# Optimization experiments

Hardware: AMD Instinct MI355X
Metric: run time of the kernel (lower is better)

## Reference

```python
import jax, jax.numpy as jnp
import numpy as np

MAX_SPAN_WIDTH = 15
NEG_INF = -10000.0


def setup_inputs() -> dict:
    key = jax.random.key(0)
    k1, k2, k3 = jax.random.split(key, 3)
    B, N = 256, 8192
    token_scores = jax.random.normal(k1, (B, N), dtype=jnp.float32)
    attention_mask = jax.random.randint(k2, (B, N), 0, 2, dtype=jnp.int32)
    width_logits = jax.random.normal(k3, (MAX_SPAN_WIDTH,), dtype=jnp.float32)
    gamma = jnp.ones((1,), dtype=jnp.float32)
    return {"token_scores": token_scores, "attention_mask": attention_mask,
            "width_logits": width_logits, "gamma": gamma}


def reference(token_scores, attention_mask, width_logits, gamma):
    B, N = token_scores.shape
    masked = jnp.where(attention_mask == 0, jnp.float32(NEG_INF), token_scores)
    width_weights = jax.nn.softmax(width_logits)  # [MAX_SPAN_WIDTH]
    boost = masked  # width-1 "boost" is the masked scores themselves
    for width in range(2, min(MAX_SPAN_WIDTH + 1, N + 1)):
        # sliding-window min over each width-`width` span -> [B, N-width+1]
        span_mins = jax.lax.reduce_window(
            masked, jnp.inf, jax.lax.min,
            window_dimensions=(1, width), window_strides=(1, 1), padding='VALID')
        w_idx = min(width - 2, MAX_SPAN_WIDTH - 1)
        weighted = span_mins * width_weights[w_idx]
        # max over all offsets a token participates in == sliding-window max
        # over weighted span-mins padded with NEG_INF (matches F.pad(value=NEG_INF))
        padded = jnp.pad(weighted, ((0, 0), (width - 1, width - 1)),
                         constant_values=NEG_INF)  # [B, N+width-1]
        expanded = jax.lax.reduce_window(
            padded, -jnp.inf, jax.lax.max,
            window_dimensions=(1, width), window_strides=(1, 1), padding='VALID')  # [B, N]
        boost = jnp.maximum(boost, expanded)
    return token_scores + gamma * boost
```

## Files before the change

kernel.cpp:

```cpp
#include <hip/hip_runtime.h>
#include <math.h>

#define TPB 256
#define TOK 4
#define TILE (TPB * TOK)
#define HALO 14
#define WIN (TOK + 2 * HALO)
#define NEGINF (-10000.0f)
#define SENT (-1.0e30f)

template <int W>
__device__ __forceinline__ void do_width(const float (&A)[WIN], float wt,
                                         float &b0, float &b1, float &b2,
                                         float &b3) {
  constexpr int K = (W < 4) ? 2 : ((W < 8) ? 4 : 8);
  float Q[W + 3];
#pragma unroll
  for (int u = 0; u < W + 3; ++u) {
    const int s = (HALO + 1) - W + u;
    if constexpr (W == K)
      Q[u] = A[s];
    else
      Q[u] = fminf(A[s], A[s + (W - K)]);
  }
  float m0, m1, m2, m3;
  if constexpr (W == 2) {
    m0 = fmaxf(Q[0], Q[1]);
    m1 = fmaxf(Q[1], Q[2]);
    m2 = fmaxf(Q[2], Q[3]);
    m3 = fmaxf(Q[3], Q[4]);
  } else if constexpr (W == 3) {
    m0 = fmaxf(Q[0], fmaxf(Q[1], Q[2]));
    m1 = fmaxf(Q[1], fmaxf(Q[2], Q[3]));
    m2 = fmaxf(Q[2], fmaxf(Q[3], Q[4]));
    m3 = fmaxf(Q[3], fmaxf(Q[4], Q[5]));
  } else {
    float core = Q[3];
#pragma unroll
    for (int u = 4; u < W; ++u) core = fmaxf(core, Q[u]);
    const float q2c = fmaxf(Q[2], core);
    const float dW = fmaxf(Q[W], Q[W + 1]);
    m0 = fmaxf(fmaxf(Q[0], Q[1]), q2c);
    m1 = fmaxf(fmaxf(Q[1], Q[W]), q2c);
    m2 = fmaxf(q2c, dW);
    m3 = fmaxf(fmaxf(core, Q[W + 2]), dW);
  }
  b0 = fmaxf(b0, m0 * wt);
  b1 = fmaxf(b1, m1 * wt);
  b2 = fmaxf(b2, m2 * wt);
  b3 = fmaxf(b3, m3 * wt);
}

__global__ __launch_bounds__(TPB, 5) void span_kernel(
    const float *__restrict__ ts, const int *__restrict__ mask,
    const float *__restrict__ wlog, const float *__restrict__ gamma_p,
    float *__restrict__ out, int N, int tiles_per_row) {
  __shared__ __align__(16) float sm[TILE + 2 * HALO];
  __shared__ float swt[15];
  const int tid = threadIdx.x;
  const int row = blockIdx.x / tiles_per_row;
  const int t0 = (blockIdx.x % tiles_per_row) * TILE;
  const float *tsrow = ts + (size_t)row * N;
  const int *mrow = mask + (size_t)row * N;

  const int j = tid * TOK;
  const int g = t0 + j;
  const int4 mv = *reinterpret_cast<const int4 *>(&mrow[g]);
  const float4 tv = *reinterpret_cast<const float4 *>(&tsrow[g]);
  {
    float2 w01, w23;
    w01.x = mv.x ? tv.x : NEGINF;
    w01.y = mv.y ? tv.y : NEGINF;
    w23.x = mv.z ? tv.z : NEGINF;
    w23.y = mv.w ? tv.w : NEGINF;
    *reinterpret_cast<float2 *>(&sm[HALO + j]) = w01;
    *reinterpret_cast<float2 *>(&sm[HALO + j + 2]) = w23;
  }
  if (tid < HALO) {
    const int gl = t0 - HALO + tid;
    sm[tid] = (gl >= 0) ? (mrow[gl] ? tsrow[gl] : NEGINF) : SENT;
    const int gr = t0 + TILE + tid;
    sm[TILE + HALO + tid] = (gr < N) ? (mrow[gr] ? tsrow[gr] : NEGINF) : SENT;
  }
  if (tid == TPB - 1) {
    float e[15], mx = -3.4e38f;
#pragma unroll
    for (int i = 0; i < 15; ++i) {
      e[i] = wlog[i];
      mx = fmaxf(mx, e[i]);
    }
    float ssum = 0.0f;
#pragma unroll
    for (int i = 0; i < 15; ++i) {
      e[i] = expf(e[i] - mx);
      ssum += e[i];
    }
    const float inv = 1.0f / ssum;
#pragma unroll
    for (int i = 0; i < 14; ++i) swt[i] = e[i] * inv;
    swt[14] = *gamma_p;
  }
  __syncthreads();

  float A[WIN];
#pragma unroll
  for (int q = 0; q < WIN / 4; ++q) {
    const float4 v = *reinterpret_cast<const float4 *>(&sm[j + 4 * q]);
    A[4 * q + 0] = v.x;
    A[4 * q + 1] = v.y;
    A[4 * q + 2] = v.z;
    A[4 * q + 3] = v.w;
  }
  float b0 = A[HALO + 0], b1 = A[HALO + 1], b2 = A[HALO + 2], b3 = A[HALO + 3];

#pragma unroll
  for (int x = 0; x < WIN - 1; ++x) A[x] = fminf(A[x], A[x + 1]);
  do_width<2>(A, swt[0], b0, b1, b2, b3);
  do_width<3>(A, swt[1], b0, b1, b2, b3);

#pragma unroll
  for (int x = 0; x < WIN - 3; ++x) A[x] = fminf(A[x], A[x + 2]);
  do_width<4>(A, swt[2], b0, b1, b2, b3);
  do_width<5>(A, swt[3], b0, b1, b2, b3);
  do_width<6>(A, swt[4], b0, b1, b2, b3);
  do_width<7>(A, swt[5], b0, b1, b2, b3);

#pragma unroll
  for (int x = 0; x < WIN - 7; ++x) A[x] = fminf(A[x], A[x + 4]);
  do_width<8>(A, swt[6], b0, b1, b2, b3);
  do_width<9>(A, swt[7], b0, b1, b2, b3);
  do_width<10>(A, swt[8], b0, b1, b2, b3);
  do_width<11>(A, swt[9], b0, b1, b2, b3);
  do_width<12>(A, swt[10], b0, b1, b2, b3);
  do_width<13>(A, swt[11], b0, b1, b2, b3);
  do_width<14>(A, swt[12], b0, b1, b2, b3);
  do_width<15>(A, swt[13], b0, b1, b2, b3);

  const float gamma = swt[14];
  float4 o;
  o.x = tv.x + gamma * b0;
  o.y = tv.y + gamma * b1;
  o.z = tv.z + gamma * b2;
  o.w = tv.w + gamma * b3;
  *reinterpret_cast<float4 *>(&out[(size_t)row * N + g]) = o;
}

extern "C" void kernel_launch(void *const *d_in, const int *in_sizes, int n_in,
                              void *d_out, int out_size, void *d_ws,
                              size_t ws_size, hipStream_t stream) {
  const float *ts = (const float *)d_in[0];
  const int *mask = (const int *)d_in[1];
  const float *wlog = (const float *)d_in[2];
  const float *gamma_p = (const float *)d_in[3];
  float *out = (float *)d_out;
  const int N = 8192;
  const int B = in_sizes[0] / N;
  const int tiles = N / TILE;
  span_kernel<<<dim3(B * tiles), dim3(TPB), 0, stream>>>(ts, mask, wlog,
                                                         gamma_p, out, N,
                                                         tiles);
}
```

Before: 14.78 us.

## Swizzle LDS tile, compute softmax weights per-wave via shuffles and readlane

Applies an XOR swizzle to the shared-memory tile indices so the float4 window reads from LDS avoid bank conflicts, padding the buffer to hold the swizzled layout. The softmax over width logits is now computed redundantly by every wave using cross-lane shuffles, and the weights are broadcast with readlane instead of being staged in shared memory by a single thread. This removes a serial single-thread loop and the LDS reads of weights on the critical path. Halo loading is merged into one branch over 28 threads, and launch bounds drop from 5 to 4 waves per SIMD, which may change register allocation and occupancy.

```diff
diff --git a/kernel.cpp b/kernel.cpp
--- a/kernel.cpp
+++ b/kernel.cpp
@@ -8,6 +8,9 @@
 #define WIN (TOK + 2 * HALO)
 #define NEGINF (-10000.0f)
 #define SENT (-1.0e30f)
+#define LDSF 1056
+
+__device__ __forceinline__ int swz(int f) { return f ^ (((f >> 5) & 7) << 2); }
 
 template <int W>
 __device__ __forceinline__ void do_width(const float (&A)[WIN], float wt,
@@ -51,12 +54,13 @@
   b3 = fmaxf(b3, m3 * wt);
 }
 
-__global__ __launch_bounds__(TPB, 5) void span_kernel(
+#define WT(W) __int_as_float(__builtin_amdgcn_readlane(wbits, (W) - 2))
+
+__global__ __launch_bounds__(TPB, 4) void span_kernel(
     const float *__restrict__ ts, const int *__restrict__ mask,
     const float *__restrict__ wlog, const float *__restrict__ gamma_p,
     float *__restrict__ out, int N, int tiles_per_row) {
-  __shared__ __align__(16) float sm[TILE + 2 * HALO];
-  __shared__ float swt[15];
+  __shared__ __align__(16) float sm[LDSF];
   const int tid = threadIdx.x;
   const int row = blockIdx.x / tiles_per_row;
   const int t0 = (blockIdx.x % tiles_per_row) * TILE;
@@ -73,39 +77,39 @@
     w01.y = mv.y ? tv.y : NEGINF;
     w23.x = mv.z ? tv.z : NEGINF;
     w23.y = mv.w ? tv.w : NEGINF;
-    *reinterpret_cast<float2 *>(&sm[HALO + j]) = w01;
-    *reinterpret_cast<float2 *>(&sm[HALO + j + 2]) = w23;
+    const int f0 = HALO + j;
+    *reinterpret_cast<float2 *>(&sm[swz(f0)]) = w01;
+    *reinterpret_cast<float2 *>(&sm[swz(f0 + 2)]) = w23;
   }
-  if (tid < HALO) {
-    const int gl = t0 - HALO + tid;
-    sm[tid] = (gl >= 0) ? (mrow[gl] ? tsrow[gl] : NEGINF) : SENT;
-    const int gr = t0 + TILE + tid;
-    sm[TILE + HALO + tid] = (gr < N) ? (mrow[gr] ? tsrow[gr] : NEGINF) : SENT;
+  if (tid < 2 * HALO) {
+    const int hk = (tid < HALO) ? tid : (TILE + tid);
+    const int tok = t0 - HALO + hk;
+    float v = SENT;
+    if (tok >= 0 && tok < N) v = mrow[tok] ? tsrow[tok] : NEGINF;
+    sm[swz(hk)] = v;
   }
-  if (tid == TPB - 1) {
-    float e[15], mx = -3.4e38f;
+
+  unsigned wbits;
+  {
+    const int li = tid & 15;
+    float v = (li < 15) ? wlog[li] : -3.4e38f;
+    float mx = v;
 #pragma unroll
-    for (int i = 0; i < 15; ++i) {
-      e[i] = wlog[i];
-      mx = fmaxf(mx, e[i]);
-    }
-    float ssum = 0.0f;
+    for (int m = 1; m < 16; m <<= 1) mx = fmaxf(mx, __shfl_xor(mx, m, 64));
+    const float e = expf(v - mx);
+    float s = e;
 #pragma unroll
-    for (int i = 0; i < 15; ++i) {
-      e[i] = expf(e[i] - mx);
-      ssum += e[i];
-    }
-    const float inv = 1.0f / ssum;
-#pragma unroll
-    for (int i = 0; i < 14; ++i) swt[i] = e[i] * inv;
-    swt[14] = *gamma_p;
+    for (int m = 1; m < 16; m <<= 1) s += __shfl_xor(s, m, 64);
+    wbits = __float_as_uint(e / s);
   }
+  const float gamma = *gamma_p;
+
   __syncthreads();
 
   float A[WIN];
 #pragma unroll
   for (int q = 0; q < WIN / 4; ++q) {
-    const float4 v = *reinterpret_cast<const float4 *>(&sm[j + 4 * q]);
+    const float4 v = *reinterpret_cast<const float4 *>(&sm[swz(j + 4 * q)]);
     A[4 * q + 0] = v.x;
     A[4 * q + 1] = v.y;
     A[4 * q + 2] = v.z;
@@ -115,28 +119,27 @@
 
 #pragma unroll
   for (int x = 0; x < WIN - 1; ++x) A[x] = fminf(A[x], A[x + 1]);
-  do_width<2>(A, swt[0], b0, b1, b2, b3);
-  do_width<3>(A, swt[1], b0, b1, b2, b3);
+  do_width<2>(A, WT(2), b0, b1, b2, b3);
+  do_width<3>(A, WT(3), b0, b1, b2, b3);
 
 #pragma unroll
   for (int x = 0; x < WIN - 3; ++x) A[x] = fminf(A[x], A[x + 2]);
-  do_width<4>(A, swt[2], b0, b1, b2, b3);
-  do_width<5>(A, swt[3], b0, b1, b2, b3);
-  do_width<6>(A, swt[4], b0, b1, b2, b3);
-  do_width<7>(A, swt[5], b0, b1, b2, b3);
+  do_width<4>(A, WT(4), b0, b1, b2, b3);
+  do_width<5>(A, WT(5), b0, b1, b2, b3);
+  do_width<6>(A, WT(6), b0, b1, b2, b3);
+  do_width<7>(A, WT(7), b0, b1, b2, b3);
 
 #pragma unroll
   for (int x = 0; x < WIN - 7; ++x) A[x] = fminf(A[x], A[x + 4]);
-  do_width<8>(A, swt[6], b0, b1, b2, b3);
-  do_width<9>(A, swt[7], b0, b1, b2, b3);
-  do_width<10>(A, swt[8], b0, b1, b2, b3);
-  do_width<11>(A, swt[9], b0, b1, b2, b3);
-  do_width<12>(A, swt[10], b0, b1, b2, b3);
-  do_width<13>(A, swt[11], b0, b1, b2, b3);
-  do_width<14>(A, swt[12], b0, b1, b2, b3);
-  do_width<15>(A, swt[13], b0, b1, b2, b3);
+  do_width<8>(A, WT(8), b0, b1, b2, b3);
+  do_width<9>(A, WT(9), b0, b1, b2, b3);
+  do_width<10>(A, WT(10), b0, b1, b2, b3);
+  do_width<11>(A, WT(11), b0, b1, b2, b3);
+  do_width<12>(A, WT(12), b0, b1, b2, b3);
+  do_width<13>(A, WT(13), b0, b1, b2, b3);
+  do_width<14>(A, WT(14), b0, b1, b2, b3);
+  do_width<15>(A, WT(15), b0, b1, b2, b3);
 
-  const float gamma = swt[14];
   float4 o;
   o.x = tv.x + gamma * b0;
   o.y = tv.y + gamma * b1;
```

After: 15.14 us. 1.02x slower.

## Process eight tokens per thread with prefix/suffix max sharing and swizzled LDS

Applied to the files above, without the earlier changes.

Each thread now handles eight tokens instead of four, so the 28-element halo window is amortised over more outputs. The sliding max per width is rebuilt as shared suffix/prefix maxima. The LDS tile gets an XOR swizzle to avoid bank conflicts on the wider float4 reads, and occupancy is lowered to four blocks per CU. The aim is to cut redundant halo loads and min/max work per token, at the cost of more registers and half as many blocks.

```diff
diff --git a/kernel.cpp b/kernel.cpp
--- a/kernel.cpp
+++ b/kernel.cpp
@@ -2,60 +2,80 @@
 #include <math.h>
 
 #define TPB 256
-#define TOK 4
+#define TOK 8
 #define TILE (TPB * TOK)
 #define HALO 14
 #define WIN (TOK + 2 * HALO)
 #define NEGINF (-10000.0f)
 #define SENT (-1.0e30f)
+#define LDSF 2080
+
+__device__ __forceinline__ int swz(int f) { return f ^ (((f >> 5) & 7) << 2); }
 
 template <int W>
 __device__ __forceinline__ void do_width(const float (&A)[WIN], float wt,
-                                         float &b0, float &b1, float &b2,
-                                         float &b3) {
+                                         float (&b)[TOK]) {
   constexpr int K = (W < 4) ? 2 : ((W < 8) ? 4 : 8);
-  float Q[W + 3];
-#pragma unroll
-  for (int u = 0; u < W + 3; ++u) {
-    const int s = (HALO + 1) - W + u;
+  constexpr int S0 = (HALO + 1) - W;
+  constexpr int NQ = W + TOK - 1;
+  float Q[NQ];
+#pragma unroll
+  for (int u = 0; u < NQ; ++u) {
     if constexpr (W == K)
-      Q[u] = A[s];
+      Q[u] = A[S0 + u];
     else
-      Q[u] = fminf(A[s], A[s + (W - K)]);
-  }
-  float m0, m1, m2, m3;
+      Q[u] = fminf(A[S0 + u], A[S0 + u + (W - K)]);
+  }
+  float m[TOK];
   if constexpr (W == 2) {
-    m0 = fmaxf(Q[0], Q[1]);
-    m1 = fmaxf(Q[1], Q[2]);
-    m2 = fmaxf(Q[2], Q[3]);
-    m3 = fmaxf(Q[3], Q[4]);
+#pragma unroll
+    for (int k = 0; k < TOK; ++k) m[k] = fmaxf(Q[k], Q[k + 1]);
   } else if constexpr (W == 3) {
-    m0 = fmaxf(Q[0], fmaxf(Q[1], Q[2]));
-    m1 = fmaxf(Q[1], fmaxf(Q[2], Q[3]));
-    m2 = fmaxf(Q[2], fmaxf(Q[3], Q[4]));
-    m3 = fmaxf(Q[3], fmaxf(Q[4], Q[5]));
+#pragma unroll
+    for (int k = 0; k < TOK; ++k)
+      m[k] = fmaxf(fmaxf(Q[k], Q[k + 1]), Q[k + 2]);
+  } else if constexpr (W < 8) {
+    float SA[4];
+    SA[3] = Q[3];
+#pragma unroll
+    for (int k = 2; k >= 0; --k) SA[k] = fmaxf(Q[k], SA[k + 1]);
+    float TA[W];
+    TA[0] = Q[3];
+#pragma unroll
+    for (int j = 1; j < W; ++j) TA[j] = fmaxf(TA[j - 1], Q[3 + j]);
+#pragma unroll
+    for (int k = 0; k < 4; ++k) m[k] = fmaxf(SA[k], TA[k + W - 4]);
+    float SB[4];
+    SB[3] = Q[7];
+#pragma unroll
+    for (int k = 2; k >= 0; --k) SB[k] = fmaxf(Q[4 + k], SB[k + 1]);
+    float TB[W];
+    TB[0] = Q[7];
+#pragma unroll
+    for (int j = 1; j < W; ++j) TB[j] = fmaxf(TB[j - 1], Q[7 + j]);
+#pragma unroll
+    for (int k = 0; k < 4; ++k) m[4 + k] = fmaxf(SB[k], TB[k + W - 4]);
   } else {
-    float core = Q[3];
-#pragma unroll
-    for (int u = 4; u < W; ++u) core = fmaxf(core, Q[u]);
-    const float q2c = fmaxf(Q[2], core);
-    const float dW = fmaxf(Q[W], Q[W + 1]);
-    m0 = fmaxf(fmaxf(Q[0], Q[1]), q2c);
-    m1 = fmaxf(fmaxf(Q[1], Q[W]), q2c);
-    m2 = fmaxf(q2c, dW);
-    m3 = fmaxf(fmaxf(core, Q[W + 2]), dW);
-  }
-  b0 = fmaxf(b0, m0 * wt);
-  b1 = fmaxf(b1, m1 * wt);
-  b2 = fmaxf(b2, m2 * wt);
-  b3 = fmaxf(b3, m3 * wt);
+    float S[8];
+    S[7] = Q[7];
+#pragma unroll
+    for (int k = 6; k >= 0; --k) S[k] = fmaxf(Q[k], S[k + 1]);
+    float T[W];
+    T[0] = Q[7];
+#pragma unroll
+    for (int j = 1; j < W; ++j) T[j] = fmaxf(T[j - 1], Q[7 + j]);
+#pragma unroll
+    for (int k = 0; k < TOK; ++k) m[k] = fmaxf(S[k], T[k + W - 8]);
+  }
+#pragma unroll
+  for (int k = 0; k < TOK; ++k) b[k] = fmaxf(b[k], m[k] * wt);
 }
 
-__global__ __launch_bounds__(TPB, 5) void span_kernel(
+__global__ __launch_bounds__(TPB, 4) void span_kernel(
     const float *__restrict__ ts, const int *__restrict__ mask,
     const float *__restrict__ wlog, const float *__restrict__ gamma_p,
     float *__restrict__ out, int N, int tiles_per_row) {
-  __shared__ __align__(16) float sm[TILE + 2 * HALO];
+  __shared__ __align__(16) float sm[LDSF];
   __shared__ float swt[15];
   const int tid = threadIdx.x;
   const int row = blockIdx.x / tiles_per_row;
@@ -65,22 +85,33 @@
 
   const int j = tid * TOK;
   const int g = t0 + j;
-  const int4 mv = *reinterpret_cast<const int4 *>(&mrow[g]);
-  const float4 tv = *reinterpret_cast<const float4 *>(&tsrow[g]);
+  const int4 mv0 = *reinterpret_cast<const int4 *>(&mrow[g]);
+  const int4 mv1 = *reinterpret_cast<const int4 *>(&mrow[g + 4]);
+  const float4 tv0 = *reinterpret_cast<const float4 *>(&tsrow[g]);
+  const float4 tv1 = *reinterpret_cast<const float4 *>(&tsrow[g + 4]);
   {
-    float2 w01, w23;
-    w01.x = mv.x ? tv.x : NEGINF;
-    w01.y = mv.y ? tv.y : NEGINF;
-    w23.x = mv.z ? tv.z : NEGINF;
-    w23.y = mv.w ? tv.w : NEGINF;
-    *reinterpret_cast<float2 *>(&sm[HALO + j]) = w01;
-    *reinterpret_cast<float2 *>(&sm[HALO + j + 2]) = w23;
-  }
-  if (tid < HALO) {
-    const int gl = t0 - HALO + tid;
-    sm[tid] = (gl >= 0) ? (mrow[gl] ? tsrow[gl] : NEGINF) : SENT;
-    const int gr = t0 + TILE + tid;
-    sm[TILE + HALO + tid] = (gr < N) ? (mrow[gr] ? tsrow[gr] : NEGINF) : SENT;
+    const int f0 = HALO + j;
+    float2 a;
+    a.x = mv0.x ? tv0.x : NEGINF;
+    a.y = mv0.y ? tv0.y : NEGINF;
+    float4 c;
+    c.x = mv0.z ? tv0.z : NEGINF;
+    c.y = mv0.w ? tv0.w : NEGINF;
+    c.z = mv1.x ? tv1.x : NEGINF;
+    c.w = mv1.y ? tv1.y : NEGINF;
+    float2 d;
+    d.x = mv1.z ? tv1.z : NEGINF;
+    d.y = mv1.w ? tv1.w : NEGINF;
+    *reinterpret_cast<float2 *>(&sm[swz(f0)]) = a;
+    *reinterpret_cast<float4 *>(&sm[swz(f0 + 2)]) = c;
+    *reinterpret_cast<float2 *>(&sm[swz(f0 + 6)]) = d;
+  }
+  if (tid < 2 * HALO) {
+    const int hk = (tid < HALO) ? tid : (TILE + tid);
+    const int tok = t0 - HALO + hk;
+    float v = SENT;
+    if (tok >= 0 && tok < N) v = mrow[tok] ? tsrow[tok] : NEGINF;
+    sm[swz(hk)] = v;
   }
   if (tid == TPB - 1) {
     float e[15], mx = -3.4e38f;
@@ -105,44 +136,52 @@
   float A[WIN];
 #pragma unroll
   for (int q = 0; q < WIN / 4; ++q) {
-    const float4 v = *reinterpret_cast<const float4 *>(&sm[j + 4 * q]);
+    const float4 v = *reinterpret_cast<const float4 *>(&sm[swz(j + 4 * q)]);
     A[4 * q + 0] = v.x;
     A[4 * q + 1] = v.y;
     A[4 * q + 2] = v.z;
     A[4 * q + 3] = v.w;
   }
-  float b0 = A[HALO + 0], b1 = A[HALO + 1], b2 = A[HALO + 2], b3 = A[HALO + 3];
+  float b[TOK];
+#pragma unroll
+  for (int k = 0; k < TOK; ++k) b[k] = A[HALO + k];
 
 #pragma unroll
   for (int x = 0; x < WIN - 1; ++x) A[x] = fminf(A[x], A[x + 1]);
-  do_width<2>(A, swt[0], b0, b1, b2, b3);
-  do_width<3>(A, swt[1], b0, b1, b2, b3);
+  do_width<2>(A, swt[0], b);
+  do_width<3>(A, swt[1], b);
 
 #pragma unroll
   for (int x = 0; x < WIN - 3; ++x) A[x] = fminf(A[x], A[x + 2]);
-  do_width<4>(A, swt[2], b0, b1, b2, b3);
-  do_width<5>(A, swt[3], b0, b1, b2, b3);
-  do_width<6>(A, swt[4], b0, b1, b2, b3);
-  do_width<7>(A, swt[5], b0, b1, b2, b3);
+  do_width<4>(A, swt[2], b);
+  do_width<5>(A, swt[3], b);
+  do_width<6>(A, swt[4], b);
+  do_width<7>(A, swt[5], b);
 
 #pragma unroll
   for (int x = 0; x < WIN - 7; ++x) A[x] = fminf(A[x], A[x + 4]);
-  do_width<8>(A, swt[6], b0, b1, b2, b3);
-  do_width<9>(A, swt[7], b0, b1, b2, b3);
-  do_width<10>(A, swt[8], b0, b1, b2, b3);
-  do_width<11>(A, swt[9], b0, b1, b2, b3);
-  do_width<12>(A, swt[10], b0, b1, b2, b3);
-  do_width<13>(A, swt[11], b0, b1, b2, b3);
-  do_width<14>(A, swt[12], b0, b1, b2, b3);
-  do_width<15>(A, swt[13], b0, b1, b2, b3);
+  do_width<8>(A, swt[6], b);
+  do_width<9>(A, swt[7], b);
+  do_width<10>(A, swt[8], b);
+  do_width<11>(A, swt[9], b);
+  do_width<12>(A, swt[10], b);
+  do_width<13>(A, swt[11], b);
+  do_width<14>(A, swt[12], b);
+  do_width<15>(A, swt[13], b);
 
   const float gamma = swt[14];
-  float4 o;
-  o.x = tv.x + gamma * b0;
-  o.y = tv.y + gamma * b1;
-  o.z = tv.z + gamma * b2;
-  o.w = tv.w + gamma * b3;
-  *reinterpret_cast<float4 *>(&out[(size_t)row * N + g]) = o;
+  float4 o0, o1;
+  o0.x = tv0.x + gamma * b[0];
+  o0.y = tv0.y + gamma * b[1];
+  o0.z = tv0.z + gamma * b[2];
+  o0.w = tv0.w + gamma * b[3];
+  o1.x = tv1.x + gamma * b[4];
+  o1.y = tv1.y + gamma * b[5];
+  o1.z = tv1.z + gamma * b[6];
+  o1.w = tv1.w + gamma * b[7];
+  float *orow = out + (size_t)row * N + g;
+  *reinterpret_cast<float4 *>(orow) = o0;
+  *reinterpret_cast<float4 *>(orow + 4) = o1;
 }
 
 extern "C" void kernel_launch(void *const *d_in, const int *in_sizes, int n_in,
```

Measured after the change: 13.45 us, median of 2. 9.0% less time.
